# Kernel tuning notes

Hardware: AMD Instinct MI355X
Metric: run time of the kernel (lower is better)

Reference implementation:

```python
import jax, jax.numpy as jnp
from jax import lax
import numpy as np

PCR0, PCR1 = -25.6, -25.6      # point_cloud_range x/y mins
VOXX, VOXY = 0.1, 0.1          # voxel_size x/y
STRIDE = 8.0                   # bev_stride
EPS = 1e-5
RADII = dict(raw=(0.4, 0.8), c1=(0.4, 0.8), c2=(0.8, 1.2), c3=(1.2, 2.4), c4=(2.4, 4.8))
NSAMP = dict(raw=(16, 16), c1=(16, 16), c2=(16, 32), c3=(16, 32), c4=(16, 32))


def ball_query(xyz, new_xyz, radius, nsample):
    # xyz [N,3], new_xyz [M,3] -> idx [M,nsample] (first-in-index-order in-radius pts), empty mask [M]
    d2 = jnp.sum((new_xyz[:, None, :] - xyz[None, :, :]) ** 2, axis=-1)  # [M,N]
    N = xyz.shape[0]
    score = jnp.where(d2 < radius * radius, jnp.arange(N, dtype=jnp.int32)[None, :], N)
    idx = -lax.top_k(-score, nsample)[0]          # ascending: smallest valid indices first
    valid = idx < N
    first = jnp.where(valid[:, :1], idx[:, :1], 0)
    idx = jnp.where(valid, idx, first)            # duplicate first neighbor into empty slots
    return idx, ~valid[:, 0]


def mlp_bn_relu(x, W, gb):
    # shared Conv2d(1x1,bias=False)+BN2d(train stats)+ReLU over [M,S,Cin]
    h = jnp.einsum('msc,cd->msd', x, W)
    mu = h.mean(axis=(0, 1))
    var = h.var(axis=(0, 1))
    return jax.nn.relu((h - mu) * lax.rsqrt(var + EPS) * gb[0] + gb[1])


def sa_module(xyz, feats, new_xyz, radii, nsamples, W0, W1, gb0, gb1):
    # StackSAModuleMSG: per radius scale -> ball query, group xyz offsets [+feats], 2-layer MLP, max-pool
    outs = []
    for s in range(2):
        idx, empty = ball_query(xyz, new_xyz, radii[s], nsamples[s])
        g = xyz[idx] - new_xyz[:, None, :]                       # [M,S,3]
        if feats is not None:
            g = jnp.concatenate([g, feats[idx]], axis=-1)        # [M,S,3+C]
        g = jnp.where(empty[:, None, None], 0.0, g)              # empty_ball_mask -> zeros
        h = mlp_bn_relu(g, W0[s], gb0[s])
        h = mlp_bn_relu(h, W1[s], gb1[s])
        outs.append(jnp.max(h, axis=1))                          # max_pool over neighbors
    return jnp.concatenate(outs, axis=-1)


def bev_interp(bev, kp):
    # exact port of bilinear_interpolate_torch; bev [H,W,C], kp [M,3] -> [M,C]
    x = (kp[:, 0] - PCR0) / VOXX / STRIDE
    y = (kp[:, 1] - PCR1) / VOXY / STRIDE
    H, W = bev.shape[0], bev.shape[1]
    x0 = jnp.floor(x).astype(jnp.int32); x1 = x0 + 1
    y0 = jnp.floor(y).astype(jnp.int32); y1 = y0 + 1
    x0 = jnp.clip(x0, 0, W - 1); x1 = jnp.clip(x1, 0, W - 1)
    y0 = jnp.clip(y0, 0, H - 1); y1 = jnp.clip(y1, 0, H - 1)
    Ia, Ib, Ic, Id = bev[y0, x0], bev[y1, x0], bev[y0, x1], bev[y1, x1]
    wa = (x1 - x) * (y1 - y); wb = (x1 - x) * (y - y0)
    wc = (x - x0) * (y1 - y); wd = (x - x0) * (y - y0)
    return Ia * wa[:, None] + Ib * wb[:, None] + Ic * wc[:, None] + Id * wd[:, None]


def _forward(kp, raw_xyz, bev, c1_xyz, c1_feat, c2_xyz, c2_feat, c3_xyz, c3_feat, c4_xyz, c4_feat,
             raw_W0, raw_W1, raw_gb0, raw_gb1, c1_W0, c1_W1, c1_gb0, c1_gb1,
             c2_W0, c2_W1, c2_gb0, c2_gb1, c3_W0, c3_W1, c3_gb0, c3_gb1,
             c4_W0, c4_W1, c4_gb0, c4_gb1, fus_W, fus_gb):
    fl = [bev_interp(bev, kp)]
    fl.append(sa_module(raw_xyz, None, kp, RADII['raw'], NSAMP['raw'], raw_W0, raw_W1, raw_gb0, raw_gb1))
    for name, x, f, W0, W1, g0, g1 in [
            ('c1', c1_xyz, c1_feat, c1_W0, c1_W1, c1_gb0, c1_gb1),
            ('c2', c2_xyz, c2_feat, c2_W0, c2_W1, c2_gb0, c2_gb1),
            ('c3', c3_xyz, c3_feat, c3_W0, c3_W1, c3_gb0, c3_gb1),
            ('c4', c4_xyz, c4_feat, c4_W0, c4_W1, c4_gb0, c4_gb1)]:
        fl.append(sa_module(x, f, kp, RADII[name], NSAMP[name], W0, W1, g0, g1))
    h = jnp.concatenate(fl, axis=-1) @ fus_W        # [M,512] @ [512,32]
    mu = h.mean(axis=0); var = h.var(axis=0)        # Linear(bias=False)+BN1d+ReLU fusion
    return jax.nn.relu((h - mu) * lax.rsqrt(var + EPS) * fus_gb[0] + fus_gb[1])


def setup_inputs() -> dict:
    keys = iter(jax.random.split(jax.random.key(0), 80))
    lo = jnp.array([-25.6, -25.6, -2.0], jnp.float32)
    span = jnp.array([51.2, 51.2, 4.0], jnp.float32)

    def pts(n):
        return lo + span * jax.random.uniform(next(keys), (n, 3), dtype=jnp.float32)

    def w(*shape):
        return jax.random.normal(next(keys), shape, dtype=jnp.float32) / np.sqrt(shape[-2])

    def gb(c):
        g = 1.0 + 0.1 * jax.random.normal(next(keys), (2, c), dtype=jnp.float32)
        b = 0.1 * jax.random.normal(next(keys), (2, c), dtype=jnp.float32)
        return jnp.stack([g, b], axis=1)  # [scale, gamma/beta, C]

    def feat(n, c):
        return jax.random.normal(next(keys), (n, c), dtype=jnp.float32)

    return dict(
        kp=pts(2048), raw_xyz=pts(30000),
        bev=jax.random.normal(next(keys), (64, 64, 128), dtype=jnp.float32),
        c1_xyz=pts(30000), c1_feat=feat(30000, 16),
        c2_xyz=pts(16000), c2_feat=feat(16000, 32),
        c3_xyz=pts(8000), c3_feat=feat(8000, 64),
        c4_xyz=pts(4000), c4_feat=feat(4000, 64),
        raw_W0=w(2, 3, 16), raw_W1=w(2, 16, 16), raw_gb0=gb(16), raw_gb1=gb(16),
        c1_W0=w(2, 19, 16), c1_W1=w(2, 16, 16), c1_gb0=gb(16), c1_gb1=gb(16),
        c2_W0=w(2, 35, 32), c2_W1=w(2, 32, 32), c2_gb0=gb(32), c2_gb1=gb(32),
        c3_W0=w(2, 67, 64), c3_W1=w(2, 64, 64), c3_gb0=gb(64), c3_gb1=gb(64),
        c4_W0=w(2, 67, 64), c4_W1=w(2, 64, 64), c4_gb0=gb(64), c4_gb1=gb(64),
        fus_W=w(512, 32),
        fus_gb=jnp.stack([1.0 + 0.1 * jax.random.normal(next(keys), (32,), dtype=jnp.float32),
                          0.1 * jax.random.normal(next(keys), (32,), dtype=jnp.float32)]),
    )


def reference(kp, raw_xyz, bev, c1_xyz, c1_feat, c2_xyz, c2_feat, c3_xyz, c3_feat, c4_xyz, c4_feat,
              raw_W0, raw_W1, raw_gb0, raw_gb1, c1_W0, c1_W1, c1_gb0, c1_gb1,
              c2_W0, c2_W1, c2_gb0, c2_gb1, c3_W0, c3_W1, c3_gb0, c3_gb1,
              c4_W0, c4_W1, c4_gb0, c4_gb1, fus_W, fus_gb):
    return _forward(kp, raw_xyz, bev, c1_xyz, c1_feat, c2_xyz, c2_feat, c3_xyz, c3_feat, c4_xyz, c4_feat,
                    raw_W0, raw_W1, raw_gb0, raw_gb1, c1_W0, c1_W1, c1_gb0, c1_gb1,
                    c2_W0, c2_W1, c2_gb0, c2_gb1, c3_W0, c3_W1, c3_gb0, c3_gb1,
                    c4_W0, c4_W1, c4_gb0, c4_gb1, fus_W, fus_gb)
```

## Files before the change

### kernel.cpp

```cpp
#include <hip/hip_runtime.h>
#include <math.h>

#define DEV_INLINE __device__ __forceinline__

struct Cfg {
  const float* xyz;
  const float* feat;
  const float* W0;
  const float* W1;
  const float* gb0;
  const float* gb1;
  int N, S, Cfeat, C0;
  int logS, logC0;
  int colOff;
  int idxOff;
  int emptyOff;
  int statOff;
  int mmOff;
  int hIdxOff;
  int bncOff;
  int fOff;
  float r2;
};
struct AllCfg { Cfg c[10]; };

struct PairCfg {
  int N, ptsOff;
  float r2s, r2b;
  int S0, S1;
  int hIdxOff0, hIdxOff1;
  int ci0, ci1;
};
struct PairAll { PairCfg p[5]; };

struct PackCfg { const float* src; int N; int off; };
struct PackAll { PackCfg c[5]; };

struct FeatCfg { const float* feat; const float* W0; int N, C0, CF, logNCG, fOff; };
struct FeatAll { FeatCfg c[8]; };

static const int M = 2048;

DEV_INLINE unsigned fkey(float f) {
  unsigned u = __float_as_uint(f);
  return (u & 0x80000000u) ? ~u : (u | 0x80000000u);
}
DEV_INLINE float funkey(unsigned k) {
  return __uint_as_float((k & 0x80000000u) ? (k & 0x7fffffffu) : ~k);
}

DEV_INLINE void decode_tile(int b, int& ci, int& t) {
  if (b < 1536) {
    const int m = b % 3;
    ci = (m == 0) ? 5 : ((m == 1) ? 7 : 9);
    t = 512 + b / 3;
  } else {
    b -= 1536;
    ci = b % 10;
    t = b / 10;
  }
}

DEV_INLINE void decode_tile3(int b, int& ci, int& t) {
  if (b < 1536) {
    const int m = b % 6;
    const int q = b / 6;
    if (m < 2)      { ci = 7; t = 2 * q + m; }
    else if (m < 4) { ci = 9; t = 2 * q + (m - 2); }
    else            { ci = (m == 4) ? 6 : 8; t = q; }
  } else {
    b -= 1536;
    const int m = b % 7;
    const int q = b / 7;
    if (m < 5) { ci = m; t = q; }
    else       { ci = 5; t = 2 * q + (m - 5); }
  }
}

__global__ __launch_bounds__(256) void k_pack(PackAll pk, float4* __restrict__ pts4) {
  const PackCfg c = pk.c[blockIdx.y];
  const int j = blockIdx.x * 256 + threadIdx.x;
  if (j >= c.N) return;
  pts4[c.off + j] = make_float4(c.src[3 * j], c.src[3 * j + 1], c.src[3 * j + 2], 0.f);
}

__global__ __launch_bounds__(256) void k_feat(FeatAll fa, float* __restrict__ Fbuf) {
  const FeatCfg c = fa.c[blockIdx.y];
  const int NCG = c.C0 >> 2;
  const int e = blockIdx.x * 256 + threadIdx.x;
  if (e >= c.N * NCG) return;
  const int j = e >> c.logNCG;
  const int cg = e & (NCG - 1);
  const float* fr = c.feat + (size_t)j * c.CF;
  const float* w = c.W0 + 3 * c.C0 + 4 * cg;
  float ax = 0.f, ay = 0.f, az = 0.f, aw = 0.f;
  for (int ci = 0; ci < c.CF; ++ci) {
    const float x = fr[ci];
    const float4 wv = *(const float4*)(w + (size_t)ci * c.C0);
    ax += x * wv.x; ay += x * wv.y; az += x * wv.z; aw += x * wv.w;
  }
  float4 o; o.x = ax; o.y = ay; o.z = az; o.w = aw;
  *(float4*)(Fbuf + c.fOff + (size_t)j * c.C0 + 4 * cg) = o;
}

__global__ __launch_bounds__(256) void k_ballq3(PairAll pairs, const float* __restrict__ kp,
                                                const float4* __restrict__ pts4,
                                                unsigned short* __restrict__ hidx,
                                                int* __restrict__ hcnt) {
  const PairCfg pc = pairs.p[blockIdx.y];
  const int lane = threadIdx.x & 63;
  const int wave = threadIdx.x >> 6;
  const int w = blockIdx.x * 4 + wave;
  const int seg = w >> 8;
  const int kbase = (w & 255) * 8;
  const int N = pc.N;
  const int Nq = ((N / 4 + 63) / 64) * 64;
  const int start = seg * Nq;
  const int end = min(N, start + Nq);
  const float4* __restrict__ pts = pts4 + pc.ptsOff;
  const float r2s = pc.r2s, r2b = pc.r2b;
  const int S0 = pc.S0, S1 = pc.S1;
  const unsigned long long lt = (1ull << lane) - 1ull;

  float qx[8], qy[8], qz[8];
  int cnt0[8], cnt1[8];
  #pragma unroll
  for (int k = 0; k < 8; ++k) {
    qx[k] = kp[(kbase + k) * 3 + 0];
    qy[k] = kp[(kbase + k) * 3 + 1];
    qz[k] = kp[(kbase + k) * 3 + 2];
    cnt0[k] = 0; cnt1[k] = 0;
  }

  unsigned short* outA = hidx + pc.hIdxOff0 + (seg * 2048 + kbase) * S0;
  unsigned short* outB = hidx + pc.hIdxOff1 + (seg * 2048 + kbase) * S1;

  float4 p0, p1;
  {
    int j0 = start + lane;           p0 = pts[j0 < end ? j0 : end - 1];
    int j1 = start + 64 + lane;      p1 = pts[j1 < end ? j1 : end - 1];
  }
  for (int base = start; base < end; base += 64) {
    const float4 cur = p0;
    p0 = p1;
    {
      int jn = base + 128 + lane;
      p1 = pts[jn < end ? jn : end - 1];
    }
    const int j = base + lane;
    float px = cur.x;
    if (j >= end) px = 3.0e38f;
    const float py = cur.y, pz = cur.z;
    #pragma unroll
    for (int k = 0; k < 8; ++k) {
      float d2;
      {
        #pragma clang fp contract(off)
        const float dx = qx[k] - px;
        const float dy = qy[k] - py;
        const float dz = qz[k] - pz;
        d2 = (dx * dx + dy * dy) + dz * dz;
      }
      const bool in1 = d2 < r2b;
      const unsigned long long m1 = __ballot(in1);
      if (m1) {
        const bool in0 = d2 < r2s;
        const unsigned long long m0 = __ballot(in0);
        if (m0) {
          if (in0) {
            const int pos = cnt0[k] + __popcll(m0 & lt);
            if (pos < S0) outA[k * S0 + pos] = (unsigned short)j;
          }
          cnt0[k] += __popcll(m0);
        }
        if (in1) {
          const int pos = cnt1[k] + __popcll(m1 & lt);
          if (pos < S1) outB[k * S1 + pos] = (unsigned short)j;
        }
        cnt1[k] += __popcll(m1);
      }
    }
    if (((base >> 6) & 3) == 3) {
      bool done = true;
      #pragma unroll
      for (int k = 0; k < 8; ++k) done = done && (cnt0[k] >= S0) && (cnt1[k] >= S1);
      if (done) break;
    }
  }

  #pragma unroll
  for (int k = 0; k < 8; ++k) {
    if (lane == 0) {
      hcnt[(pc.ci0 * 4 + seg) * 2048 + kbase + k] = cnt0[k];
      hcnt[(pc.ci1 * 4 + seg) * 2048 + kbase + k] = cnt1[k];
    }
  }
}

__global__ __launch_bounds__(256) void k_merge(AllCfg cfgs,
                                               const unsigned short* __restrict__ hidx,
                                               const int* __restrict__ hcnt,
                                               unsigned short* __restrict__ idxbuf,
                                               int* __restrict__ emptybuf) {
  const Cfg cfg = cfgs.c[blockIdx.y];
  const int S = cfg.S;
  const int ci = (int)blockIdx.y;
  const int e = blockIdx.x * 256 + threadIdx.x;
  if (e >= 2048 * S) return;
  const int p = e & (S - 1);
  const int m = e >> cfg.logS;
  const int c0 = min(hcnt[(ci * 4 + 0) * 2048 + m], S);
  const int c1 = min(hcnt[(ci * 4 + 1) * 2048 + m], S);
  const int c2 = min(hcnt[(ci * 4 + 2) * 2048 + m], S);
  const int c3 = min(hcnt[(ci * 4 + 3) * 2048 + m], S);
  const unsigned short* A = hidx + cfg.hIdxOff + (0 * 2048 + m) * S;
  const unsigned short* B = hidx + cfg.hIdxOff + (1 * 2048 + m) * S;
  const unsigned short* C = hidx + cfg.hIdxOff + (2 * 2048 + m) * S;
  const unsigned short* D = hidx + cfg.hIdxOff + (3 * 2048 + m) * S;
  const unsigned short first = c0 ? A[0] : (c1 ? B[0] : (c2 ? C[0] : (c3 ? D[0] : (unsigned short)0)));
  unsigned short v = first;
  int rem = p;
  if (rem < c0) v = A[rem];
  else {
    rem -= c0;
    if (rem < c1) v = B[rem];
    else {
      rem -= c1;
      if (rem < c2) v = C[rem];
      else {
        rem -= c2;
        if (rem < c3) v = D[rem];
      }
    }
  }
  idxbuf[cfg.idxOff + m * S + p] = v;
  if (p == 0) emptybuf[cfg.emptyOff + m] = (c0 + c1 + c2 + c3 == 0) ? 1 : 0;
}

__global__ __launch_bounds__(256) void k_ballq(AllCfg cfgs, const float* __restrict__ kp,
                                               unsigned short* __restrict__ idxbuf,
                                               int* __restrict__ emptybuf) {
  const Cfg cfg = cfgs.c[blockIdx.y];
  const int lane = threadIdx.x & 63;
  const int wid = (blockIdx.x * blockDim.x + threadIdx.x) >> 6;
  if (wid >= M) return;
  const float qx = kp[wid * 3 + 0], qy = kp[wid * 3 + 1], qz = kp[wid * 3 + 2];
  const int N = cfg.N, S = cfg.S;
  const float r2 = cfg.r2;
  const float* __restrict__ xyz = cfg.xyz;
  unsigned short* out = idxbuf + cfg.idxOff + wid * S;
  int cnt = 0, first = -1;
  for (int base = 0; base < N; base += 64) {
    const int j = base + lane;
    bool inb = false;
    if (j < N) {
      #pragma clang fp contract(off)
      const float dx = qx - xyz[j * 3 + 0];
      const float dy = qy - xyz[j * 3 + 1];
      const float dz = qz - xyz[j * 3 + 2];
      const float d2 = (dx * dx + dy * dy) + dz * dz;
      inb = d2 < r2;
    }
    const unsigned long long msk = __ballot(inb);
    if (msk) {
      if (inb) {
        const int pos = cnt + __popcll(msk & ((1ull << lane) - 1ull));
        if (pos < S) out[pos] = (unsigned short)j;
      }
      if (first < 0) first = base + __builtin_ctzll(msk);
      cnt += __popcll(msk);
      if (cnt >= S) break;
    }
  }
  const unsigned short fillv = (unsigned short)(first < 0 ? 0 : first);
  for (int p = cnt + lane; p < S; p += 64) out[p] = fillv;
  if (lane == 0) emptybuf[cfg.emptyOff + wid] = (first < 0) ? 1 : 0;
}

template<int CIN, int S, int CPR>
DEV_INLINE void stage_rows2(const Cfg& cfg, const float* __restrict__ kp,
                            const unsigned short* __restrict__ idxbuf,
                            const int* __restrict__ emptybuf,
                            int base, float* __restrict__ in_f) {
  const int tid = threadIdx.x;
  const int r = tid >> 2, j = tid & 3;
  const int grow = base + r;
  const int m = grow >> ((S == 16) ? 4 : 5);
  const bool emp = emptybuf[cfg.emptyOff + m] != 0;
  const int idx = (int)idxbuf[cfg.idxOff + grow];
  float* dst = in_f + r * CPR;
  if (j == 0) {
    if (emp) { dst[0] = 0.f; dst[1] = 0.f; dst[2] = 0.f; }
    else {
      const float* p = cfg.xyz + 3 * idx;
      dst[0] = p[0] - kp[m * 3 + 0];
      dst[1] = p[1] - kp[m * 3 + 1];
      dst[2] = p[2] - kp[m * 3 + 2];
    }
    dst[CIN] = 0.f;
  }
  if constexpr (CIN > 3) {
    constexpr int CF4 = (CIN - 3) / 4;
    const float4* f4 = (const float4*)cfg.feat + (size_t)idx * CF4;
    for (int c = j; c < CF4; c += 4) {
      float4 v;
      if (emp) v = make_float4(0.f, 0.f, 0.f, 0.f); else v = f4[c];
      dst[3 + 4 * c] = v.x; dst[4 + 4 * c] = v.y;
      dst[5 + 4 * c] = v.z; dst[6 + 4 * c] = v.w;
    }
  }
}

__global__ __launch_bounds__(64) void k_bnc(AllCfg cfgs, const double* __restrict__ statsR,
                                            float* __restrict__ bnc, int phase) {
  const Cfg cfg = cfgs.c[blockIdx.x];
  const int cc = threadIdx.x;
  if (cc >= cfg.C0) return;
  const int off = cfg.statOff + (phase ? 128 : 0);
  double s = 0.0, q = 0.0;
  #pragma unroll
  for (int r = 0; r < 4; ++r) {
    s += statsR[r * 2560 + off + cc];
    q += statsR[r * 2560 + off + 64 + cc];
  }
  const double n = (double)(2048 * cfg.S);
  const double mu = s / n;
  const double var = q / n - mu * mu;
  const double inv = 1.0 / sqrt(var + 1e-5);
  const float* gb = phase ? cfg.gb1 : cfg.gb0;
  const double g = (double)gb[cc], b = (double)gb[cfg.C0 + cc];
  bnc[cfg.bncOff + cc] = (float)(inv * g);
  bnc[cfg.bncOff + 64 + cc] = (float)(b - mu * inv * g);
}

template<int S>
DEV_INLINE void stage_gxyz(const Cfg& cfg, const float* __restrict__ kp,
                           const unsigned short* __restrict__ idxbuf,
                           const int* __restrict__ emptybuf,
                           int tile, float4* gxl, int* idxL) {
  const int tid = threadIdx.x;
  constexpr int LOGS = (S == 16) ? 4 : 5;
  if (tid < 64) {
    const int grow = tile * 64 + tid;
    const int m = grow >> LOGS;
    const bool emp = emptybuf[cfg.emptyOff + m] != 0;
    const int idx = (int)idxbuf[cfg.idxOff + grow];
    idxL[tid] = idx;
    float4 g;
    if (emp) { g.x = 0.f; g.y = 0.f; g.z = 0.f; g.w = 0.f; }
    else {
      const float* p = cfg.xyz + 3 * idx;
      g.x = p[0] - kp[m * 3 + 0];
      g.y = p[1] - kp[m * 3 + 1];
      g.z = p[2] - kp[m * 3 + 2];
      g.w = 1.f;
    }
    gxl[tid] = g;
  }
}

template<int C0, int S, bool HASF>
DEV_INLINE void p1f_impl(const Cfg& cfg, const float* __restrict__ kp,
                         const unsigned short* __restrict__ idxbuf,
                         const int* __restrict__ emptybuf,
                         const float* __restrict__ Fb,
                         double* __restrict__ statsR, int pair, char* smem) {
  constexpr int NCG = C0 / 4;
  constexpr int RPT = (NCG / 4 < 1) ? 1 : NCG / 4;
  constexpr int LOGCG = (NCG == 4) ? 2 : ((NCG == 8) ? 3 : 4);
  float4* gxl = (float4*)smem;
  int* idxL = (int*)(smem + 1024);
  float* sA = (float*)(smem + 1280);
  float* sB = (float*)(smem + 1536);
  const int tid = threadIdx.x;
  const int cg = tid & (NCG - 1);
  const int rg = tid >> LOGCG;
  const int r0 = rg * RPT;
  const int cc0 = 4 * cg;
  const float4 wx = *(const float4*)(cfg.W0 + 0 * C0 + cc0);
  const float4 wy = *(const float4*)(cfg.W0 + 1 * C0 + cc0);
  const float4 wz = *(const float4*)(cfg.W0 + 2 * C0 + cc0);
  float ls[4] = {0.f, 0.f, 0.f, 0.f}, lq[4] = {0.f, 0.f, 0.f, 0.f};
  #pragma unroll
  for (int sub = 0; sub < 2; ++sub) {
    if (sub) __syncthreads();
    stage_gxyz<S>(cfg, kp, idxbuf, emptybuf, pair * 2 + sub, gxl, idxL);
    __syncthreads();
    #pragma unroll
    for (int rr = 0; rr < RPT; ++rr) {
      const int r = r0 + rr;
      const float4 g = gxl[r];
      float hx = g.x * wx.x + g.y * wy.x + g.z * wz.x;
      float hy = g.x * wx.y + g.y * wy.y + g.z * wz.y;
      float hz = g.x * wx.z + g.y * wy.z + g.z * wz.z;
      float hw = g.x * wx.w + g.y * wy.w + g.z * wz.w;
      if constexpr (HASF) {
        const float4 Fv = *(const float4*)(Fb + cfg.fOff + (size_t)idxL[r] * C0 + cc0);
        hx += g.w * Fv.x; hy += g.w * Fv.y; hz += g.w * Fv.z; hw += g.w * Fv.w;
      }
      ls[0] += hx; lq[0] += hx * hx;
      ls[1] += hy; lq[1] += hy * hy;
      ls[2] += hz; lq[2] += hz * hz;
      ls[3] += hw; lq[3] += hw * hw;
    }
  }
  #pragma unroll
  for (int cj = 0; cj < 4; ++cj)
    #pragma unroll
    for (int off = NCG; off < 64; off <<= 1) {
      ls[cj] += __shfl_xor(ls[cj], off);
      lq[cj] += __shfl_xor(lq[cj], off);
    }
  __syncthreads();
  if (tid < 64) { sA[tid] = 0.f; sB[tid] = 0.f; }
  __syncthreads();
  if ((tid & 63) < NCG) {
    #pragma unroll
    for (int cj = 0; cj < 4; ++cj) {
      atomicAdd(&sA[cc0 + cj], ls[cj]);
      atomicAdd(&sB[cc0 + cj], lq[cj]);
    }
  }
  __syncthreads();
  const int rep = blockIdx.x & 3;
  if (tid < C0) {
    atomicAdd(&statsR[rep * 2560 + cfg.statOff + tid], (double)sA[tid]);
    atomicAdd(&statsR[rep * 2560 + cfg.statOff + 64 + tid], (double)sB[tid]);
  }
}

__global__ __launch_bounds__(256) void k_p1f_all(AllCfg cfgs, const float* __restrict__ kp,
                                                 const unsigned short* __restrict__ idxbuf,
                                                 const int* __restrict__ emptybuf,
                                                 const float* __restrict__ Fb,
                                                 double* __restrict__ statsR) {
  __shared__ char smem[1792];
  int ci, t;
  decode_tile3(blockIdx.x, ci, t);
  switch (ci) {
    case 0: p1f_impl<16, 16, false>(cfgs.c[0], kp, idxbuf, emptybuf, Fb, statsR, t, smem); break;
    case 1: p1f_impl<16, 16, false>(cfgs.c[1], kp, idxbuf, emptybuf, Fb, statsR, t, smem); break;
    case 2: p1f_impl<16, 16, true>(cfgs.c[2], kp, idxbuf, emptybuf, Fb, statsR, t, smem); break;
    case 3: p1f_impl<16, 16, true>(cfgs.c[3], kp, idxbuf, emptybuf, Fb, statsR, t, smem); break;
    case 4: p1f_impl<32, 16, true>(cfgs.c[4], kp, idxbuf, emptybuf, Fb, statsR, t, smem); break;
    case 5: p1f_impl<32, 32, true>(cfgs.c[5], kp, idxbuf, emptybuf, Fb, statsR, t, smem); break;
    case 6: p1f_impl<64, 16, true>(cfgs.c[6], kp, idxbuf, emptybuf, Fb, statsR, t, smem); break;
    case 7: p1f_impl<64, 32, true>(cfgs.c[7], kp, idxbuf, emptybuf, Fb, statsR, t, smem); break;
    case 8: p1f_impl<64, 16, true>(cfgs.c[8], kp, idxbuf, emptybuf, Fb, statsR, t, smem); break;
    case 9: p1f_impl<64, 32, true>(cfgs.c[9], kp, idxbuf, emptybuf, Fb, statsR, t, smem); break;
  }
}

template<int C0, int S, bool HASF>
DEV_INLINE void p2f_impl(const Cfg& cfg, const float* __restrict__ kp,
                         const unsigned short* __restrict__ idxbuf,
                         const int* __restrict__ emptybuf,
                         const float* __restrict__ Fb,
                         double* __restrict__ statsR,
                         const float* __restrict__ bnc0,
                         float* __restrict__ maxbuf, float* __restrict__ minbuf,
                         int pair, char* smem) {
  constexpr int NCG = C0 / 4;
  constexpr int RPT = (NCG / 4 < 1) ? 1 : NCG / 4;
  constexpr int CPR = C0 + 4;
  constexpr int LOGCG = (NCG == 4) ? 2 : ((NCG == 8) ? 3 : 4);
  constexpr int LOGS = (S == 16) ? 4 : 5;
  constexpr int NM = 64 / S;
  float* a0 = (float*)smem;
  float4* gxl = (float4*)(smem + 17408);
  int* idxL = (int*)(smem + 18432);
  unsigned* mxl = (unsigned*)(smem + 18688);
  unsigned* mnl = (unsigned*)(smem + 19712);
  const int tid = threadIdx.x;
  const int cg = tid & (NCG - 1);
  const int rg = tid >> LOGCG;
  const int r0 = rg * RPT;
  const int cc0 = 4 * cg;
  const float4 wx = *(const float4*)(cfg.W0 + 0 * C0 + cc0);
  const float4 wy = *(const float4*)(cfg.W0 + 1 * C0 + cc0);
  const float4 wz = *(const float4*)(cfg.W0 + 2 * C0 + cc0);
  const float4 scv = *(const float4*)(bnc0 + cfg.bncOff + cc0);
  const float4 shv = *(const float4*)(bnc0 + cfg.bncOff + 64 + cc0);
  float ls[4] = {0.f, 0.f, 0.f, 0.f}, lq[4] = {0.f, 0.f, 0.f, 0.f};

  #pragma unroll
  for (int sub = 0; sub < 2; ++sub) {
    const int tile64 = pair * 2 + sub;
    if (sub) __syncthreads();
    stage_gxyz<S>(cfg, kp, idxbuf, emptybuf, tile64, gxl, idxL);
    if (tid < NM * C0) { mxl[tid] = 0u; mnl[tid] = 0xFFFFFFFFu; }
    __syncthreads();
    #pragma unroll
    for (int rr = 0; rr < RPT; ++rr) {
      const int r = r0 + rr;
      const float4 g = gxl[r];
      float hx = g.x * wx.x + g.y * wy.x + g.z * wz.x;
      float hy = g.x * wx.y + g.y * wy.y + g.z * wz.y;
      float hz = g.x * wx.z + g.y * wy.z + g.z * wz.z;
      float hw = g.x * wx.w + g.y * wy.w + g.z * wz.w;
      if constexpr (HASF) {
        const float4 Fv = *(const float4*)(Fb + cfg.fOff + (size_t)idxL[r] * C0 + cc0);
        hx += g.w * Fv.x; hy += g.w * Fv.y; hz += g.w * Fv.z; hw += g.w * Fv.w;
      }
      float4 o;
      o.x = fmaxf(hx * scv.x + shv.x, 0.f);
      o.y = fmaxf(hy * scv.y + shv.y, 0.f);
      o.z = fmaxf(hz * scv.z + shv.z, 0.f);
      o.w = fmaxf(hw * scv.w + shv.w, 0.f);
      *(float4*)(a0 + r * CPR + cc0) = o;
    }
    __syncthreads();
    float acc1[RPT][4];
    #pragma unroll
    for (int rr = 0; rr < RPT; ++rr)
      acc1[rr][0] = acc1[rr][1] = acc1[rr][2] = acc1[rr][3] = 0.f;
    const float* W1g = cfg.W1 + cc0;
    #pragma unroll 2
    for (int c4 = 0; c4 < C0 / 4; ++c4) {
      const float4 w0 = *(const float4*)(W1g + (4 * c4 + 0) * C0);
      const float4 w1 = *(const float4*)(W1g + (4 * c4 + 1) * C0);
      const float4 w2 = *(const float4*)(W1g + (4 * c4 + 2) * C0);
      const float4 w3 = *(const float4*)(W1g + (4 * c4 + 3) * C0);
      #pragma unroll
      for (int rr = 0; rr < RPT; ++rr) {
        const float4 a = *(const float4*)(a0 + (r0 + rr) * CPR + 4 * c4);
        acc1[rr][0] += a.x * w0.x + a.y * w1.x + a.z * w2.x + a.w * w3.x;
        acc1[rr][1] += a.x * w0.y + a.y * w1.y + a.z * w2.y + a.w * w3.y;
        acc1[rr][2] += a.x * w0.z + a.y * w1.z + a.z * w2.z + a.w * w3.z;
        acc1[rr][3] += a.x * w0.w + a.y * w1.w + a.z * w2.w + a.w * w3.w;
      }
    }
    #pragma unroll
    for (int cj = 0; cj < 4; ++cj) {
      float s = 0.f, q = 0.f;
      unsigned kmax = 0u, kmin = 0xFFFFFFFFu;
      #pragma unroll
      for (int rr = 0; rr < RPT; ++rr) {
        const float v = acc1[rr][cj];
        s += v; q += v * v;
        const unsigned kk = fkey(v);
        kmax = kmax > kk ? kmax : kk;
        kmin = kmin < kk ? kmin : kk;
      }
      ls[cj] += s; lq[cj] += q;
      const int cell = (r0 >> LOGS) * C0 + cc0 + cj;
      atomicMax(&mxl[cell], kmax);
      atomicMin(&mnl[cell], kmin);
    }
    __syncthreads();
    if (tid < NM * C0) {
      const int gcell = ((tile64 * 64) >> LOGS) * C0 + tid;
      maxbuf[cfg.mmOff + gcell] = funkey(mxl[tid]);
      minbuf[cfg.mmOff + gcell] = funkey(mnl[tid]);
    }
  }
  __syncthreads();
  float* sA = (float*)smem;
  float* sB = sA + 64;
  #pragma unroll
  for (int cj = 0; cj < 4; ++cj)
    #pragma unroll
    for (int off = NCG; off < 64; off <<= 1) {
      ls[cj] += __shfl_xor(ls[cj], off);
      lq[cj] += __shfl_xor(lq[cj], off);
    }
  if (tid < 64) { sA[tid] = 0.f; sB[tid] = 0.f; }
  __syncthreads();
  if ((tid & 63) < NCG) {
    #pragma unroll
    for (int cj = 0; cj < 4; ++cj) {
      atomicAdd(&sA[cc0 + cj], ls[cj]);
      atomicAdd(&sB[cc0 + cj], lq[cj]);
    }
  }
  __syncthreads();
  const int rep = blockIdx.x & 3;
  if (tid < C0) {
    atomicAdd(&statsR[rep * 2560 + cfg.statOff + 128 + tid], (double)sA[tid]);
    atomicAdd(&statsR[rep * 2560 + cfg.statOff + 192 + tid], (double)sB[tid]);
  }
}

__global__ __launch_bounds__(256) void k_p2f_all(AllCfg cfgs, const float* __restrict__ kp,
                                                 const unsigned short* __restrict__ idxbuf,
                                                 const int* __restrict__ emptybuf,
                                                 const float* __restrict__ Fb,
                                                 double* __restrict__ statsR,
                                                 const float* __restrict__ bnc0,
                                                 float* __restrict__ maxbuf,
                                                 float* __restrict__ minbuf) {
  __shared__ char smem[20736];
  int ci, t;
  decode_tile3(blockIdx.x, ci, t);
  switch (ci) {
    case 0: p2f_impl<16, 16, false>(cfgs.c[0], kp, idxbuf, emptybuf, Fb, statsR, bnc0, maxbuf, minbuf, t, smem); break;
    case 1: p2f_impl<16, 16, false>(cfgs.c[1], kp, idxbuf, emptybuf, Fb, statsR, bnc0, maxbuf, minbuf, t, smem); break;
    case 2: p2f_impl<16, 16, true>(cfgs.c[2], kp, idxbuf, emptybuf, Fb, statsR, bnc0, maxbuf, minbuf, t, smem); break;
    case 3: p2f_impl<16, 16, true>(cfgs.c[3], kp, idxbuf, emptybuf, Fb, statsR, bnc0, maxbuf, minbuf, t, smem); break;
    case 4: p2f_impl<32, 16, true>(cfgs.c[4], kp, idxbuf, emptybuf, Fb, statsR, bnc0, maxbuf, minbuf, t, smem); break;
    case 5: p2f_impl<32, 32, true>(cfgs.c[5], kp, idxbuf, emptybuf, Fb, statsR, bnc0, maxbuf, minbuf, t, smem); break;
    case 6: p2f_impl<64, 16, true>(cfgs.c[6], kp, idxbuf, emptybuf, Fb, statsR, bnc0, maxbuf, minbuf, t, smem); break;
    case 7: p2f_impl<64, 32, true>(cfgs.c[7], kp, idxbuf, emptybuf, Fb, statsR, bnc0, maxbuf, minbuf, t, smem); break;
    case 8: p2f_impl<64, 16, true>(cfgs.c[8], kp, idxbuf, emptybuf, Fb, statsR, bnc0, maxbuf, minbuf, t, smem); break;
    case 9: p2f_impl<64, 32, true>(cfgs.c[9], kp, idxbuf, emptybuf, Fb, statsR, bnc0, maxbuf, minbuf, t, smem); break;
  }
}

template<int C0, int CIN, int S>
__device__ __forceinline__ void p1_impl(const Cfg& cfg, const float* __restrict__ kp,
                                        const unsigned short* __restrict__ idxbuf,
                                        const int* __restrict__ emptybuf,
                                        double* __restrict__ statsR, int tile, char* smem) {
  constexpr int CPD = CIN + 1;
  constexpr int CPR = (C0 == 16) ? 20 : (CPD > C0 ? CPD : C0);
  constexpr int NCG = C0 / 4;
  constexpr int RPT = NCG / 4;
  constexpr int RPTc = (RPT < 1) ? 1 : RPT;
  constexpr int LOGCG = (NCG == 4) ? 2 : ((NCG == 8) ? 3 : 4);
  float* in_f = (float*)smem;
  const int tid = threadIdx.x;
  stage_rows2<CIN, S, CPR>(cfg, kp, idxbuf, emptybuf, tile * 64, in_f);
  const int cg = tid & (NCG - 1);
  const int rg = tid >> LOGCG;
  const int r0 = rg * RPTc;
  const int cc0 = 4 * cg;
  __syncthreads();
  float acc[RPTc][4];
  #pragma unroll
  for (int rr = 0; rr < RPTc; ++rr)
    acc[rr][0] = acc[rr][1] = acc[rr][2] = acc[rr][3] = 0.f;
  const float* W0g = cfg.W0 + cc0;
  #pragma unroll 2
  for (int c4 = 0; c4 < CIN / 4; ++c4) {
    const float4 w0 = *(const float4*)(W0g + (4 * c4 + 0) * C0);
    const float4 w1 = *(const float4*)(W0g + (4 * c4 + 1) * C0);
    const float4 w2 = *(const float4*)(W0g + (4 * c4 + 2) * C0);
    const float4 w3 = *(const float4*)(W0g + (4 * c4 + 3) * C0);
    #pragma unroll
    for (int rr = 0; rr < RPTc; ++rr) {
      const float4 a = *(const float4*)(in_f + (r0 + rr) * CPR + 4 * c4);
      acc[rr][0] += a.x * w0.x + a.y * w1.x + a.z * w2.x + a.w * w3.x;
      acc[rr][1] += a.x * w0.y + a.y * w1.y + a.z * w2.y + a.w * w3.y;
      acc[rr][2] += a.x * w0.z + a.y * w1.z + a.z * w2.z + a.w * w3.z;
      acc[rr][3] += a.x * w0.w + a.y * w1.w + a.z * w2.w + a.w * w3.w;
    }
  }
  {
    constexpr int ci0 = (CIN / 4) * 4;
    const float4 w0 = *(const float4*)(W0g + (ci0 + 0) * C0);
    const float4 w1 = *(const float4*)(W0g + (ci0 + 1) * C0);
    const float4 w2 = *(const float4*)(W0g + (ci0 + 2) * C0);
    #pragma unroll
    for (int rr = 0; rr < RPTc; ++rr) {
      const float4 a = *(const float4*)(in_f + (r0 + rr) * CPR + ci0);
      acc[rr][0] += a.x * w0.x + a.y * w1.x + a.z * w2.x;
      acc[rr][1] += a.x * w0.y + a.y * w1.y + a.z * w2.y;
      acc[rr][2] += a.x * w0.z + a.y * w1.z + a.z * w2.z;
      acc[rr][3] += a.x * w0.w + a.y * w1.w + a.z * w2.w;
    }
  }
  float ls[4], lq[4];
  #pragma unroll
  for (int cj = 0; cj < 4; ++cj) {
    float s = 0.f, q = 0.f;
    #pragma unroll
    for (int rr = 0; rr < RPTc; ++rr) { s += acc[rr][cj]; q += acc[rr][cj] * acc[rr][cj]; }
    ls[cj] = s; lq[cj] = q;
  }
  __syncthreads();
  float* sA = (float*)smem;
  float* sB = sA + 64;
  #pragma unroll
  for (int cj = 0; cj < 4; ++cj)
    #pragma unroll
    for (int off = NCG; off < 64; off <<= 1) {
      ls[cj] += __shfl_xor(ls[cj], off);
      lq[cj] += __shfl_xor(lq[cj], off);
    }
  if (tid < 64) { sA[tid] = 0.f; sB[tid] = 0.f; }
  __syncthreads();
  if ((tid & 63) < NCG) {
    #pragma unroll
    for (int cj = 0; cj < 4; ++cj) {
      atomicAdd(&sA[cc0 + cj], ls[cj]);
      atomicAdd(&sB[cc0 + cj], lq[cj]);
    }
  }
  __syncthreads();
  const int rep = blockIdx.x & 3;
  if (tid < C0) {
    atomicAdd(&statsR[rep * 2560 + cfg.statOff + tid], (double)sA[tid]);
    atomicAdd(&statsR[rep * 2560 + cfg.statOff + 64 + tid], (double)sB[tid]);
  }
}

__global__ __launch_bounds__(256) void k_p1_all(AllCfg cfgs, const float* __restrict__ kp,
                                                const unsigned short* __restrict__ idxbuf,
                                                const int* __restrict__ emptybuf,
                                                double* __restrict__ statsR) {
  __shared__ char smem[17408];
  int ci, t;
  decode_tile(blockIdx.x, ci, t);
  switch (ci) {
    case 0: p1_impl<16, 3, 16>(cfgs.c[0], kp, idxbuf, emptybuf, statsR, t, smem); break;
    case 1: p1_impl<16, 3, 16>(cfgs.c[1], kp, idxbuf, emptybuf, statsR, t, smem); break;
    case 2: p1_impl<16, 19, 16>(cfgs.c[2], kp, idxbuf, emptybuf, statsR, t, smem); break;
    case 3: p1_impl<16, 19, 16>(cfgs.c[3], kp, idxbuf, emptybuf, statsR, t, smem); break;
    case 4: p1_impl<32, 35, 16>(cfgs.c[4], kp, idxbuf, emptybuf, statsR, t, smem); break;
    case 5: p1_impl<32, 35, 32>(cfgs.c[5], kp, idxbuf, emptybuf, statsR, t, smem); break;
    case 6: p1_impl<64, 67, 16>(cfgs.c[6], kp, idxbuf, emptybuf, statsR, t, smem); break;
    case 7: p1_impl<64, 67, 32>(cfgs.c[7], kp, idxbuf, emptybuf, statsR, t, smem); break;
    case 8: p1_impl<64, 67, 16>(cfgs.c[8], kp, idxbuf, emptybuf, statsR, t, smem); break;
    case 9: p1_impl<64, 67, 32>(cfgs.c[9], kp, idxbuf, emptybuf, statsR, t, smem); break;
  }
}

template<int C0, int CIN, int S>
__device__ __forceinline__ void p2_impl(const Cfg& cfg, const float* __restrict__ kp,
                                        const unsigned short* __restrict__ idxbuf,
                                        const int* __restrict__ emptybuf,
                                        double* __restrict__ statsR,
                                        const float* __restrict__ bnc0,
                                        float* __restrict__ maxbuf,
                                        float* __restrict__ minbuf, int tile, char* smem) {
  constexpr int CPD = CIN + 1;
  constexpr int CPR = (C0 == 16) ? 20 : (CPD > C0 ? CPD : C0);
  constexpr int NCG = C0 / 4;
  constexpr int RPT = NCG / 4;
  constexpr int RPTc = (RPT < 1) ? 1 : RPT;
  constexpr int LOGCG = (NCG == 4) ? 2 : ((NCG == 8) ? 3 : 4);
  constexpr int LOGS = (S == 16) ? 4 : 5;
  constexpr int NM = 64 / S;
  float* in_f = (float*)smem;
  unsigned* mxl = (unsigned*)(smem + 17408);
  unsigned* mnl = mxl + 256;
  const int tid = threadIdx.x;
  stage_rows2<CIN, S, CPR>(cfg, kp, idxbuf, emptybuf, tile * 64, in_f);
  if (tid < NM * C0) { mxl[tid] = 0u; mnl[tid] = 0xFFFFFFFFu; }
  const int cg = tid & (NCG - 1);
  const int rg = tid >> LOGCG;
  const int r0 = rg * RPTc;
  const int cc0 = 4 * cg;
  __syncthreads();
  float acc[RPTc][4];
  #pragma unroll
  for (int rr = 0; rr < RPTc; ++rr)
// ... 351 lines not shown
  const int k = e & 31;
  const double n = 2048.0;
  const double* st = stats + 2560;
  const double mu = st[k] / n;
  const double v = st[32 + k] / n - mu * mu;
  const double inv = 1.0 / sqrt(v + 1e-5);
  const double g = (double)fgb[k], b = (double)fgb[32 + k];
  out[e] = fmaxf((float)(inv * g) * hbuf[e] + (float)(b - mu * inv * g), 0.f);
}

extern "C" void kernel_launch(void* const* d_in, const int* in_sizes, int n_in,
                              void* d_out, int out_size, void* d_ws, size_t ws_size,
                              hipStream_t stream) {
  (void)in_sizes; (void)n_in; (void)out_size;

  const float* kp   = (const float*)d_in[0];
  const float* raw  = (const float*)d_in[1];
  const float* bev  = (const float*)d_in[2];
  const float* c1x  = (const float*)d_in[3];
  const float* c1f  = (const float*)d_in[4];
  const float* c2x  = (const float*)d_in[5];
  const float* c2f  = (const float*)d_in[6];
  const float* c3x  = (const float*)d_in[7];
  const float* c3f  = (const float*)d_in[8];
  const float* c4x  = (const float*)d_in[9];
  const float* c4f  = (const float*)d_in[10];
  const float* fusW = (const float*)d_in[31];
  const float* fgb  = (const float*)d_in[32];

  char* ws = (char*)d_ws;
  double* stats = (double*)ws;
  float* bnc0   = (float*)(ws + 21504);
  float* bnc1   = (float*)(ws + 26624);
  unsigned short* idxbuf = (unsigned short*)(ws + 32768);
  int* emptybuf = (int*)(ws + 32768 + 1310720);
  float* fused  = (float*)(ws + 1425408);
  double* statsR = (double*)(ws + 1425408 + 4194304);
  float* hbuf   = (float*)(ws + 1425408 + 4194304);
  float* maxbuf = (float*)(ws + 5881856);
  float* minbuf = (float*)(ws + 9027584);
  float4* pts4  = (float4*)(ws + 12173312);
  int* hcnt = (int*)(ws + 5881856);
  unsigned short* hidx = (unsigned short*)(ws + 5881856 + 327680);
  float* Fbuf = (float*)(ws + 13581312);
  const size_t need_old = 5881856;
  const size_t need_new = 12173312;
  const size_t need_bq2 = 13581312;
  const size_t need_F  = 13581312 + 14080000ull;
  if (ws_size < need_old) return;
  const bool fast = (ws_size >= need_new);
  const bool bq3 = (ws_size >= need_bq2) && fast;
  const bool Fp = (ws_size >= need_F) && bq3;

  AllCfg cfgs;
  int mmCum = 0, hCum = 0, fCum = 0;
  auto setCfg = [&](int i, const float* xyz, const float* feat, int N, int Cf, int C0, int S,
                    double r, const float* W0b, const float* W1b, const float* g0b,
                    const float* g1b, int sIdx, int col) {
    Cfg& c = cfgs.c[i];
    const int Cin = 3 + Cf;
    c.xyz = xyz; c.feat = feat;
    c.W0 = W0b + (size_t)sIdx * Cin * C0;
    c.W1 = W1b + (size_t)sIdx * C0 * C0;
    c.gb0 = g0b + (size_t)sIdx * 2 * C0;
    c.gb1 = g1b + (size_t)sIdx * 2 * C0;
    c.N = N; c.S = S; c.Cfeat = Cf; c.C0 = C0;
    c.logS = (S == 16) ? 4 : 5;
    c.logC0 = (C0 == 16) ? 4 : ((C0 == 32) ? 5 : 6);
    c.colOff = col;
    c.idxOff = i * 65536;
    c.emptyOff = i * 2048;
    c.statOff = i * 256;
    c.mmOff = mmCum;
    mmCum += 2048 * C0;
    c.hIdxOff = hCum;
    hCum += 4 * 2048 * S;
    c.bncOff = i * 128;
    c.fOff = (Cf > 0) ? fCum : 0;
    if (Cf > 0) fCum += N * C0;
    c.r2 = (float)(r * r);
  };

  const float* rW0 = (const float*)d_in[11]; const float* rW1 = (const float*)d_in[12];
  const float* rg0 = (const float*)d_in[13]; const float* rg1 = (const float*)d_in[14];
  const float* aW0 = (const float*)d_in[15]; const float* aW1 = (const float*)d_in[16];
  const float* ag0 = (const float*)d_in[17]; const float* ag1 = (const float*)d_in[18];
  const float* bW0 = (const float*)d_in[19]; const float* bW1 = (const float*)d_in[20];
  const float* bg0 = (const float*)d_in[21]; const float* bg1 = (const float*)d_in[22];
  const float* cW0 = (const float*)d_in[23]; const float* cW1 = (const float*)d_in[24];
  const float* cg0 = (const float*)d_in[25]; const float* cg1 = (const float*)d_in[26];
  const float* dW0 = (const float*)d_in[27]; const float* dW1 = (const float*)d_in[28];
  const float* dg0 = (const float*)d_in[29]; const float* dg1 = (const float*)d_in[30];

  setCfg(0, raw, nullptr, 30000,  0, 16, 16, 0.4, rW0, rW1, rg0, rg1, 0, 128);
  setCfg(1, raw, nullptr, 30000,  0, 16, 16, 0.8, rW0, rW1, rg0, rg1, 1, 144);
  setCfg(2, c1x, c1f,     30000, 16, 16, 16, 0.4, aW0, aW1, ag0, ag1, 0, 160);
  setCfg(3, c1x, c1f,     30000, 16, 16, 16, 0.8, aW0, aW1, ag0, ag1, 1, 176);
  setCfg(4, c2x, c2f,     16000, 32, 32, 16, 0.8, bW0, bW1, bg0, bg1, 0, 192);
  setCfg(5, c2x, c2f,     16000, 32, 32, 32, 1.2, bW0, bW1, bg0, bg1, 1, 224);
  setCfg(6, c3x, c3f,      8000, 64, 64, 16, 1.2, cW0, cW1, cg0, cg1, 0, 256);
  setCfg(7, c3x, c3f,      8000, 64, 64, 32, 2.4, cW0, cW1, cg0, cg1, 1, 320);
  setCfg(8, c4x, c4f,      4000, 64, 64, 16, 2.4, dW0, dW1, dg0, dg1, 0, 384);
  setCfg(9, c4x, c4f,      4000, 64, 64, 32, 4.8, dW0, dW1, dg0, dg1, 1, 448);

  hipMemsetAsync(stats, 0, 2624 * sizeof(double), stream);
  if (fast) hipMemsetAsync(statsR, 0, 4 * 2560 * sizeof(double), stream);

  if (Fp) {
    FeatAll fa;
    for (int k = 0; k < 8; ++k) {
      const Cfg& c = cfgs.c[2 + k];
      fa.c[k].feat = c.feat;
      fa.c[k].W0 = c.W0;
      fa.c[k].N = c.N;
      fa.c[k].C0 = c.C0;
      fa.c[k].CF = c.Cfeat;
      fa.c[k].logNCG = (c.C0 == 16) ? 2 : ((c.C0 == 32) ? 3 : 4);
      fa.c[k].fOff = c.fOff;
    }
    k_feat<<<dim3(500, 8), 256, 0, stream>>>(fa, Fbuf);
  }

  if (bq3) {
    PackAll pk;
    pk.c[0] = { raw, 30000, 0 };
    pk.c[1] = { c1x, 30000, 30000 };
    pk.c[2] = { c2x, 16000, 60000 };
    pk.c[3] = { c3x,  8000, 76000 };
    pk.c[4] = { c4x,  4000, 84000 };
    PairAll pr;
    auto setPair = [&](int p, int ci0, int ci1, int N, int off) {
      PairCfg& q = pr.p[p];
      q.N = N; q.ptsOff = off;
      q.r2s = cfgs.c[ci0].r2; q.r2b = cfgs.c[ci1].r2;
      q.S0 = cfgs.c[ci0].S;   q.S1 = cfgs.c[ci1].S;
      q.hIdxOff0 = cfgs.c[ci0].hIdxOff; q.hIdxOff1 = cfgs.c[ci1].hIdxOff;
      q.ci0 = ci0; q.ci1 = ci1;
    };
    setPair(0, 0, 1, 30000, 0);
    setPair(1, 2, 3, 30000, 30000);
    setPair(2, 4, 5, 16000, 60000);
    setPair(3, 6, 7,  8000, 76000);
    setPair(4, 8, 9,  4000, 84000);
    k_pack<<<dim3(118, 5), 256, 0, stream>>>(pk, pts4);
    k_ballq3<<<dim3(256, 5), 256, 0, stream>>>(pr, kp, pts4, hidx, hcnt);
    k_merge<<<dim3(256, 10), 256, 0, stream>>>(cfgs, hidx, hcnt, idxbuf, emptybuf);
  } else {
    k_ballq<<<dim3(512, 10), 256, 0, stream>>>(cfgs, kp, idxbuf, emptybuf);
  }

  k_bev<<<dim3(1024), 256, 0, stream>>>(kp, bev, fused);
  if (fast) {
    if (Fp) {
      k_p1f_all<<<dim3(3328), 256, 0, stream>>>(cfgs, kp, idxbuf, emptybuf, Fbuf, statsR);
      k_bnc<<<dim3(10), 64, 0, stream>>>(cfgs, statsR, bnc0, 0);
      k_p2f_all<<<dim3(3328), 256, 0, stream>>>(cfgs, kp, idxbuf, emptybuf, Fbuf, statsR, bnc0, maxbuf, minbuf);
    } else {
      k_p1_all<<<dim3(6656), 256, 0, stream>>>(cfgs, kp, idxbuf, emptybuf, statsR);
      k_bnc<<<dim3(10), 64, 0, stream>>>(cfgs, statsR, bnc0, 0);
      k_p2_all<<<dim3(6656), 256, 0, stream>>>(cfgs, kp, idxbuf, emptybuf, statsR, bnc0, maxbuf, minbuf);
    }
    k_bnc<<<dim3(10), 64, 0, stream>>>(cfgs, statsR, bnc1, 1);
    k_fin<<<dim3(512, 10), 256, 0, stream>>>(cfgs, bnc1, maxbuf, minbuf, fused);
  } else {
    k_stats0<<<dim3(256, 10), 256, 0, stream>>>(cfgs, kp, idxbuf, emptybuf, stats);
    k_stats1<<<dim3(512, 10), 256, 0, stream>>>(cfgs, kp, idxbuf, emptybuf, stats);
    k_final<<<dim3(2048, 10), 256, 0, stream>>>(cfgs, kp, idxbuf, emptybuf, stats, fused);
  }
  k_fus_mm<<<dim3(256), 256, 0, stream>>>(fused, fusW, hbuf, stats);
  k_fus_out<<<dim3(256), 256, 0, stream>>>(hbuf, stats, fgb, (float*)d_out);
}
```

Measured before the change: 217.2 us.

## Double-buffer gxyz staging and process four tiles per block in p1f/p2f

Each block of the fused p1f and p2f kernels now handles four 64-row tiles instead of two, and the grid is halved to match. The grouped-xyz and index staging is double-buffered in shared memory, so the next tile loads while the current one is computed, and one barrier per tile replaces two. This cuts block count and per-block setup (weight loads, stats atomics) and hides staging latency. In exchange it uses more shared memory, gives fewer blocks for load balance, and p2f now resets the max/min buffers every tile.

```diff
diff --git a/kernel.cpp b/kernel.cpp
--- a/kernel.cpp
+++ b/kernel.cpp
@@ -61,15 +61,15 @@
   }
 }
 
-DEV_INLINE void decode_tile3(int b, int& ci, int& t) {
-  if (b < 1536) {
+DEV_INLINE void decode_tile4(int b, int& ci, int& t) {
+  if (b < 768) {
     const int m = b % 6;
     const int q = b / 6;
     if (m < 2)      { ci = 7; t = 2 * q + m; }
     else if (m < 4) { ci = 9; t = 2 * q + (m - 2); }
     else            { ci = (m == 4) ? 6 : 8; t = q; }
   } else {
-    b -= 1536;
+    b -= 768;
     const int m = b % 7;
     const int q = b / 7;
     if (m < 5) { ci = m; t = q; }
@@ -364,14 +364,16 @@
                          const unsigned short* __restrict__ idxbuf,
                          const int* __restrict__ emptybuf,
                          const float* __restrict__ Fb,
-                         double* __restrict__ statsR, int pair, char* smem) {
+                         double* __restrict__ statsR, int quad, char* smem) {
   constexpr int NCG = C0 / 4;
   constexpr int RPT = (NCG / 4 < 1) ? 1 : NCG / 4;
   constexpr int LOGCG = (NCG == 4) ? 2 : ((NCG == 8) ? 3 : 4);
-  float4* gxl = (float4*)smem;
-  int* idxL = (int*)(smem + 1024);
-  float* sA = (float*)(smem + 1280);
-  float* sB = (float*)(smem + 1536);
+  float4* gx0 = (float4*)smem;
+  float4* gx1 = (float4*)(smem + 1024);
+  int* id0 = (int*)(smem + 2048);
+  int* id1 = (int*)(smem + 2304);
+  float* sA = (float*)(smem + 2560);
+  float* sB = (float*)(smem + 2816);
   const int tid = threadIdx.x;
   const int cg = tid & (NCG - 1);
   const int rg = tid >> LOGCG;
@@ -381,21 +383,26 @@
   const float4 wy = *(const float4*)(cfg.W0 + 1 * C0 + cc0);
   const float4 wz = *(const float4*)(cfg.W0 + 2 * C0 + cc0);
   float ls[4] = {0.f, 0.f, 0.f, 0.f}, lq[4] = {0.f, 0.f, 0.f, 0.f};
-  #pragma unroll
-  for (int sub = 0; sub < 2; ++sub) {
-    if (sub) __syncthreads();
-    stage_gxyz<S>(cfg, kp, idxbuf, emptybuf, pair * 2 + sub, gxl, idxL);
-    __syncthreads();
+  stage_gxyz<S>(cfg, kp, idxbuf, emptybuf, quad * 4 + 0, gx0, id0);
+  __syncthreads();
+  #pragma unroll
+  for (int sub = 0; sub < 4; ++sub) {
+    float4* gcur = (sub & 1) ? gx1 : gx0;
+    int* icur = (sub & 1) ? id1 : id0;
+    float4* gnx = (sub & 1) ? gx0 : gx1;
+    int* inx = (sub & 1) ? id0 : id1;
+    if (sub < 3)
+      stage_gxyz<S>(cfg, kp, idxbuf, emptybuf, quad * 4 + sub + 1, gnx, inx);
     #pragma unroll
     for (int rr = 0; rr < RPT; ++rr) {
       const int r = r0 + rr;
-      const float4 g = gxl[r];
+      const float4 g = gcur[r];
       float hx = g.x * wx.x + g.y * wy.x + g.z * wz.x;
       float hy = g.x * wx.y + g.y * wy.y + g.z * wz.y;
       float hz = g.x * wx.z + g.y * wy.z + g.z * wz.z;
       float hw = g.x * wx.w + g.y * wy.w + g.z * wz.w;
       if constexpr (HASF) {
-        const float4 Fv = *(const float4*)(Fb + cfg.fOff + (size_t)idxL[r] * C0 + cc0);
+        const float4 Fv = *(const float4*)(Fb + cfg.fOff + (size_t)icur[r] * C0 + cc0);
         hx += g.w * Fv.x; hy += g.w * Fv.y; hz += g.w * Fv.z; hw += g.w * Fv.w;
       }
       ls[0] += hx; lq[0] += hx * hx;
@@ -403,6 +410,7 @@
       ls[2] += hz; lq[2] += hz * hz;
       ls[3] += hw; lq[3] += hw * hw;
     }
+    __syncthreads();
   }
   #pragma unroll
   for (int cj = 0; cj < 4; ++cj)
@@ -411,7 +419,6 @@
       ls[cj] += __shfl_xor(ls[cj], off);
       lq[cj] += __shfl_xor(lq[cj], off);
     }
-  __syncthreads();
   if (tid < 64) { sA[tid] = 0.f; sB[tid] = 0.f; }
   __syncthreads();
   if ((tid & 63) < NCG) {
@@ -434,9 +441,9 @@
                                                  const int* __restrict__ emptybuf,
                                                  const float* __restrict__ Fb,
                                                  double* __restrict__ statsR) {
-  __shared__ char smem[1792];
+  __shared__ char smem[3072];
   int ci, t;
-  decode_tile3(blockIdx.x, ci, t);
+  decode_tile4(blockIdx.x, ci, t);
   switch (ci) {
     case 0: p1f_impl<16, 16, false>(cfgs.c[0], kp, idxbuf, emptybuf, Fb, statsR, t, smem); break;
     case 1: p1f_impl<16, 16, false>(cfgs.c[1], kp, idxbuf, emptybuf, Fb, statsR, t, smem); break;
@@ -459,7 +466,7 @@
                          double* __restrict__ statsR,
                          const float* __restrict__ bnc0,
                          float* __restrict__ maxbuf, float* __restrict__ minbuf,
-                         int pair, char* smem) {
+                         int quad, char* smem) {
   constexpr int NCG = C0 / 4;
   constexpr int RPT = (NCG / 4 < 1) ? 1 : NCG / 4;
   constexpr int CPR = C0 + 4;
@@ -467,10 +474,12 @@
   constexpr int LOGS = (S == 16) ? 4 : 5;
   constexpr int NM = 64 / S;
   float* a0 = (float*)smem;
-  float4* gxl = (float4*)(smem + 17408);
-  int* idxL = (int*)(smem + 18432);
-  unsigned* mxl = (unsigned*)(smem + 18688);
-  unsigned* mnl = (unsigned*)(smem + 19712);
+  float4* gx0 = (float4*)(smem + 17408);
+  float4* gx1 = (float4*)(smem + 18432);
+  int* id0 = (int*)(smem + 19456);
+  int* id1 = (int*)(smem + 19712);
+  unsigned* mxl = (unsigned*)(smem + 19968);
+  unsigned* mnl = (unsigned*)(smem + 20992);
   const int tid = threadIdx.x;
   const int cg = tid & (NCG - 1);
   const int rg = tid >> LOGCG;
@@ -483,23 +492,29 @@
   const float4 shv = *(const float4*)(bnc0 + cfg.bncOff + 64 + cc0);
   float ls[4] = {0.f, 0.f, 0.f, 0.f}, lq[4] = {0.f, 0.f, 0.f, 0.f};
 
-  #pragma unroll
-  for (int sub = 0; sub < 2; ++sub) {
-    const int tile64 = pair * 2 + sub;
-    if (sub) __syncthreads();
-    stage_gxyz<S>(cfg, kp, idxbuf, emptybuf, tile64, gxl, idxL);
-    if (tid < NM * C0) { mxl[tid] = 0u; mnl[tid] = 0xFFFFFFFFu; }
-    __syncthreads();
+  stage_gxyz<S>(cfg, kp, idxbuf, emptybuf, quad * 4 + 0, gx0, id0);
+  if (tid < NM * C0) { mxl[tid] = 0u; mnl[tid] = 0xFFFFFFFFu; }
+  __syncthreads();
+
+  #pragma unroll
+  for (int sub = 0; sub < 4; ++sub) {
+    float4* gcur = (sub & 1) ? gx1 : gx0;
+    int* icur = (sub & 1) ? id1 : id0;
+    float4* gnx = (sub & 1) ? gx0 : gx1;
+    int* inx = (sub & 1) ? id0 : id1;
+    const int tile64 = quad * 4 + sub;
+    if (sub < 3)
+      stage_gxyz<S>(cfg, kp, idxbuf, emptybuf, tile64 + 1, gnx, inx);
     #pragma unroll
     for (int rr = 0; rr < RPT; ++rr) {
       const int r = r0 + rr;
-      const float4 g = gxl[r];
+      const float4 g = gcur[r];
       float hx = g.x * wx.x + g.y * wy.x + g.z * wz.x;
       float hy = g.x * wx.y + g.y * wy.y + g.z * wz.y;
       float hz = g.x * wx.z + g.y * wy.z + g.z * wz.z;
       float hw = g.x * wx.w + g.y * wy.w + g.z * wz.w;
       if constexpr (HASF) {
-        const float4 Fv = *(const float4*)(Fb + cfg.fOff + (size_t)idxL[r] * C0 + cc0);
+        const float4 Fv = *(const float4*)(Fb + cfg.fOff + (size_t)icur[r] * C0 + cc0);
         hx += g.w * Fv.x; hy += g.w * Fv.y; hz += g.w * Fv.z; hw += g.w * Fv.w;
       }
       float4 o;
@@ -552,9 +567,10 @@
       const int gcell = ((tile64 * 64) >> LOGS) * C0 + tid;
       maxbuf[cfg.mmOff + gcell] = funkey(mxl[tid]);
       minbuf[cfg.mmOff + gcell] = funkey(mnl[tid]);
-    }
-  }
-  __syncthreads();
+      mxl[tid] = 0u; mnl[tid] = 0xFFFFFFFFu;
+    }
+    __syncthreads();
+  }
   float* sA = (float*)smem;
   float* sB = sA + 64;
   #pragma unroll
@@ -589,9 +605,9 @@
                                                  const float* __restrict__ bnc0,
                                                  float* __restrict__ maxbuf,
                                                  float* __restrict__ minbuf) {
-  __shared__ char smem[20736];
+  __shared__ char smem[22016];
   int ci, t;
-  decode_tile3(blockIdx.x, ci, t);
+  decode_tile4(blockIdx.x, ci, t);
   switch (ci) {
     case 0: p2f_impl<16, 16, false>(cfgs.c[0], kp, idxbuf, emptybuf, Fb, statsR, bnc0, maxbuf, minbuf, t, smem); break;
     case 1: p2f_impl<16, 16, false>(cfgs.c[1], kp, idxbuf, emptybuf, Fb, statsR, bnc0, maxbuf, minbuf, t, smem); break;
@@ -1249,9 +1265,9 @@
   k_bev<<<dim3(1024), 256, 0, stream>>>(kp, bev, fused);
   if (fast) {
     if (Fp) {
-      k_p1f_all<<<dim3(3328), 256, 0, stream>>>(cfgs, kp, idxbuf, emptybuf, Fbuf, statsR);
+      k_p1f_all<<<dim3(1664), 256, 0, stream>>>(cfgs, kp, idxbuf, emptybuf, Fbuf, statsR);
       k_bnc<<<dim3(10), 64, 0, stream>>>(cfgs, statsR, bnc0, 0);
-      k_p2f_all<<<dim3(3328), 256, 0, stream>>>(cfgs, kp, idxbuf, emptybuf, Fbuf, statsR, bnc0, maxbuf, minbuf);
+      k_p2f_all<<<dim3(1664), 256, 0, stream>>>(cfgs, kp, idxbuf, emptybuf, Fbuf, statsR, bnc0, maxbuf, minbuf);
     } else {
       k_p1_all<<<dim3(6656), 256, 0, stream>>>(cfgs, kp, idxbuf, emptybuf, statsR);
       k_bnc<<<dim3(10), 64, 0, stream>>>(cfgs, statsR, bnc0, 0);
```

Result: slower. 228.7 us (+5.3%).
